# Optimization experiments

Measured on AMD Instinct MI355X. Metric: run time of the kernel, lower is better.

## Reference

```python
import jax, jax.numpy as jnp
import numpy as np
from jax import lax

L = 4096          # sequence length (timesteps)
N_ITEMS = 512     # number of items == RNN input_size (x[:,:,k] is (L, N))
HIDDEN = 256
NUM_LAYERS = 16
NUM_FEATURES = 4
OUT_SIZE = 2


def _rnn_params(key, input_size):
    """Vanilla tanh RNN params, PyTorch-style uniform(-1/sqrt(H), 1/sqrt(H))."""
    ks = jax.random.split(key, 5)
    s = 1.0 / np.sqrt(HIDDEN)
    u = lambda k, shape: jax.random.uniform(k, shape, jnp.float32, -s, s)
    return dict(
        Wih0=u(ks[0], (HIDDEN, input_size)),              # layer 0 input weights
        Wih=u(ks[1], (NUM_LAYERS - 1, HIDDEN, HIDDEN)),   # layers 1..15 input weights
        Whh=u(ks[2], (NUM_LAYERS, HIDDEN, HIDDEN)),
        bih=u(ks[3], (NUM_LAYERS, HIDDEN)),
        bhh=u(ks[4], (NUM_LAYERS, HIDDEN)),
    )


def setup_inputs() -> dict:
    key = jax.random.key(0)
    kx, k1, k2, k3 = jax.random.split(key, 4)
    x = jax.random.normal(kx, (L, N_ITEMS, NUM_FEATURES), jnp.float32)
    lp = _rnn_params(k1, N_ITEMS)    # self.low_price (used for features 0, 2, 3)
    lpv = _rnn_params(k2, N_ITEMS)   # self.low_price_vol (used for feature 1)
    kf1, kf2 = jax.random.split(k3)
    s = 1.0 / np.sqrt(HIDDEN * NUM_FEATURES)
    fc_W = jax.random.uniform(kf1, (OUT_SIZE, HIDDEN * NUM_FEATURES), jnp.float32, -s, s)
    fc_b = jax.random.uniform(kf2, (OUT_SIZE,), jnp.float32, -s, s)
    return {
        "x": x,
        "lp_Wih0": lp["Wih0"], "lp_Wih": lp["Wih"], "lp_Whh": lp["Whh"],
        "lp_bih": lp["bih"], "lp_bhh": lp["bhh"],
        "lpv_Wih0": lpv["Wih0"], "lpv_Wih": lpv["Wih"], "lpv_Whh": lpv["Whh"],
        "lpv_bih": lpv["bih"], "lpv_bhh": lpv["bhh"],
        "fc_W": fc_W, "fc_b": fc_b,
    }


def _run_rnn(seq, Wih0, Wih, Whh, bih, bhh):
    """Multi-layer vanilla tanh RNN over an unbatched (L, input_size) sequence.
    Returns the top-layer hidden state at the last timestep, shape (HIDDEN,)."""

    def step(h, x_t):  # h: (NUM_LAYERS, HIDDEN); x_t: (input_size,)
        inp = jnp.tanh(Wih0 @ x_t + bih[0] + Whh[0] @ h[0] + bhh[0])
        hs = [inp]
        for l in range(1, NUM_LAYERS):
            inp = jnp.tanh(Wih[l - 1] @ inp + bih[l] + Whh[l] @ h[l] + bhh[l])
            hs.append(inp)
        return jnp.stack(hs), None

    h0 = jnp.zeros((NUM_LAYERS, HIDDEN), seq.dtype)
    h_final, _ = lax.scan(step, h0, seq)
    return h_final[-1]


def reference(x, lp_Wih0, lp_Wih, lp_Whh, lp_bih, lp_bhh,
              lpv_Wih0, lpv_Wih, lpv_Whh, lpv_bih, lpv_bhh, fc_W, fc_b):
    lp = (lp_Wih0, lp_Wih, lp_Whh, lp_bih, lp_bhh)
    lpv = (lpv_Wih0, lpv_Wih, lpv_Whh, lpv_bih, lpv_bhh)
    # Faithful to the original (buggy) forward: low_price for features 0,2,3;
    # low_price_vol for feature 1.
    h0 = _run_rnn(x[:, :, 0], *lp)
    h1 = _run_rnn(x[:, :, 1], *lpv)
    h2 = _run_rnn(x[:, :, 2], *lp)
    h3 = _run_rnn(x[:, :, 3], *lp)
    out = jnp.concatenate([h0, h1, h2, h3])  # (4*HIDDEN,)
    return fc_W @ out + fc_b  # (OUT_SIZE,)
```

## Files before the change

kernel.cpp:

```cpp
#include <hip/hip_runtime.h>
#include <hip/hip_bf16.h>
#include <math.h>

#define SEQL   4096
#define NITEMS 512
#define HID    256
#define NLAY   16
#define QS     64
#define CHUNK  8
#define NCHUNK (SEQL / CHUNK)
#define TPB    4

typedef float f4 __attribute__((ext_vector_type(4)));

#define P_OFF   ((size_t)0)
#define H_OFF   (P_OFF + (size_t)4*SEQL*HID)
#define AP_OFF  (H_OFF + (size_t)4*NLAY*QS*HID)
#define HF_OFF  (AP_OFF + (size_t)4*NLAY*QS*HID)
#define FLAG_OFF_FLOATS (HF_OFF + (size_t)1024)
#define NFLAGS 256

__device__ __forceinline__ f4 ld_coh_f4(const float* p) {
    f4 r;
    asm volatile("global_load_dwordx4 %0, %1, off sc0 sc1" : "=v"(r) : "v"(p));
    return r;
}
__device__ __forceinline__ float ld_coh_b32(const float* p) {
    float r;
    asm volatile("global_load_dword %0, %1, off sc0 sc1" : "=v"(r) : "v"(p));
    return r;
}
__device__ __forceinline__ void st_coh_b32(float* p, float v) {
    asm volatile("global_store_dword %0, %1, off sc0 sc1" :: "v"(p), "v"(v) : "memory");
}
__device__ __forceinline__ void st_coh_u32(unsigned* p, unsigned v) {
    asm volatile("global_store_dword %0, %1, off sc0 sc1" :: "v"(p), "v"(v) : "memory");
}
__device__ __forceinline__ unsigned uload(const unsigned* p) {
    return __hip_atomic_load(p, __ATOMIC_RELAXED, __HIP_MEMORY_SCOPE_AGENT);
}

#define SBAR()  { __builtin_amdgcn_s_barrier(); __builtin_amdgcn_sched_barrier(0); }
#define LGKM0() { asm volatile("s_waitcnt lgkmcnt(0)" ::: "memory"); __builtin_amdgcn_sched_barrier(0); }
#define VMW0()  { asm volatile("s_waitcnt vmcnt(0)" ::: "memory"); __builtin_amdgcn_sched_barrier(0); }

__device__ __forceinline__ void spin_ge(const unsigned* p, unsigned target, bool* dead) {
    if (*dead) return;
    unsigned it = 0;
    while (uload(p) < target) {
        __builtin_amdgcn_s_sleep(1);
        if (++it > (1u << 20)) { *dead = true; break; }
    }
}

__device__ __forceinline__ float tanh_fast(float x) {
    return 1.f - __fdividef(2.f, __expf(2.f * x) + 1.f);
}

#define FMAC0(ACC, HB, W) \
    asm volatile("v_fmac_f32 %0, %1, %2" : "+v"(ACC) : "v"(HB), "v"(W));
#define FMACR(ACC, HB, W, I) \
    asm volatile("v_fmac_f32_dpp %0, %1, %2 row_ror:" #I " row_mask:0xf bank_mask:0xf" \
                 : "+v"(ACC) : "v"(HB), "v"(W));

#define FMAC_BLOCK(HB, WB) \
    FMAC0(acc0, HB, w[WB+0])      FMACR(acc1, HB, w[WB+1], 1)   \
    FMACR(acc2, HB, w[WB+2], 2)   FMACR(acc3, HB, w[WB+3], 3)   \
    FMACR(acc0, HB, w[WB+4], 4)   FMACR(acc1, HB, w[WB+5], 5)   \
    FMACR(acc2, HB, w[WB+6], 6)   FMACR(acc3, HB, w[WB+7], 7)   \
    FMACR(acc0, HB, w[WB+8], 8)   FMACR(acc1, HB, w[WB+9], 9)   \
    FMACR(acc2, HB, w[WB+10], 10) FMACR(acc3, HB, w[WB+11], 11) \
    FMACR(acc0, HB, w[WB+12], 12) FMACR(acc1, HB, w[WB+13], 13) \
    FMACR(acc2, HB, w[WB+14], 14) FMACR(acc3, HB, w[WB+15], 15)

__global__ __launch_bounds__(1024) void proj_kernel(
    const float* __restrict__ x, const float* __restrict__ Wlp,
    const float* __restrict__ Wlpv, float* __restrict__ P)
{
    __shared__ float xs[TPB][4][NITEMS];
    const int tid = threadIdx.x;
    const int t0 = blockIdx.x * TPB;

    #pragma unroll
    for (int tt = 0; tt < TPB; ++tt) {
        const float2* src = (const float2*)(x + (size_t)(t0 + tt) * NITEMS * 4);
        float2 v = src[tid];
        int e = 2 * tid;
        xs[tt][e & 3][e >> 2]       = v.x;
        xs[tt][(e + 1) & 3][e >> 2] = v.y;
    }
    __syncthreads();

    const int c = tid >> 8, j = tid & 255;
    const float* W = (c == 1) ? Wlpv : Wlp;
    const float4* row = (const float4*)(W + (size_t)j * NITEMS);
    float acc[TPB] = {0.f, 0.f, 0.f, 0.f};
    #pragma unroll 4
    for (int k4 = 0; k4 < NITEMS / 4; ++k4) {
        float4 w = row[k4];
        #pragma unroll
        for (int tt = 0; tt < TPB; ++tt) {
            float4 xv = *(const float4*)(&xs[tt][c][k4 * 4]);
            acc[tt] = fmaf(w.x, xv.x, fmaf(w.y, xv.y, fmaf(w.z, xv.z, fmaf(w.w, xv.w, acc[tt]))));
        }
    }
    #pragma unroll
    for (int tt = 0; tt < TPB; ++tt)
        P[((size_t)c * SEQL + (t0 + tt)) * HID + j] = acc[tt];
}

__global__ __launch_bounds__(1024) void rnn_pipe(
    const float* __restrict__ lp_Wih,  const float* __restrict__ lp_Whh,
    const float* __restrict__ lp_bih,  const float* __restrict__ lp_bhh,
    const float* __restrict__ lpv_Wih, const float* __restrict__ lpv_Whh,
    const float* __restrict__ lpv_bih, const float* __restrict__ lpv_bhh,
    const float* __restrict__ P, float* __restrict__ Hring,
    float* __restrict__ Apart, float* __restrict__ hfinal,
    unsigned* __restrict__ Hflag, unsigned* __restrict__ Aflag)
{
    __shared__ __align__(16) float part2[2][1024];
    __shared__ __align__(16) float hvec[HID];
    __shared__ __align__(16) float hstage[CHUNK * HID];
    __shared__ float ldspad[18000];

    const int b = blockIdx.x;
    if (b >= 124) return;
    const int tid = threadIdx.x;
    ldspad[tid] = 0.f;

    const int c = b / 31;
    const int r = b % 31;
    const int role = (r < NLAY) ? 0 : 1;
    const int l = (r < NLAY) ? r : (r - NLAY + 1);

    const float* Wih = (c == 1) ? lpv_Wih : lp_Wih;
    const float* Whh = (c == 1) ? lpv_Whh : lp_Whh;
    const float* bih = (c == 1) ? lpv_bih : lp_bih;
    const float* bhh = (c == 1) ? lpv_bhh : lp_bhh;

    const int j    = tid & 255;
    const int c4   = tid >> 8;
    const int lane = tid & 63;
    const int q    = lane & 15;
    const int m    = (c4 << 6) | lane;
    const int gbase = (c4 << 6) | q;
    const bool first = ((tid & 192) == 0);
    bool dead = false;

    if (role == 0) {
        const bool l0 = (l == 0);

        float w[64];
        {
            const float* Wrow = Whh + ((size_t)l * HID + j) * HID;
            #pragma unroll
            for (int bb = 0; bb < 4; ++bb)
                #pragma unroll
                for (int i = 0; i < 16; ++i)
                    w[bb * 16 + i] = Wrow[(c4 << 6) + bb * 16 + ((q - i) & 15)];
        }
        #pragma unroll
        for (int i = 0; i < 64; ++i) asm volatile("" : "+v"(w[i]));

        float bias_m = 0.f;
        if (first) bias_m = bih[l * HID + m] + bhh[l * HID + m];

        const float*    Psrc  = P + (size_t)c * SEQL * HID;
        const float*    apbuf = Apart + ((size_t)(c * NLAY + l) * QS) * HID;
        const unsigned* af    = Aflag + c * NLAY + l;
        unsigned*       myHfl = Hflag + c * NLAY + l;
        const unsigned* consA = Aflag + c * NLAY + l + 1;
        float*          Hout  = Hring + ((size_t)(c * NLAY + l) * QS) * HID;
        float*          hfin  = hfinal + (size_t)c * HID;

        float hb0 = 0.f, hb1 = 0.f, hb2 = 0.f, hb3 = 0.f;

        for (int k = 0; k < NCHUNK; ++k) {
            if (tid == 0) {
                if (!l0) spin_ge(af, (unsigned)(k + 1), &dead);
                if (l < NLAY - 1 && k >= CHUNK) spin_ge(consA, (unsigned)(k - 7), &dead);
            }
            SBAR();
            float ap8[CHUNK];
            if (first) {
                if (l0) {
                    #pragma unroll
                    for (int s = 0; s < CHUNK; ++s)
                        ap8[s] = Psrc[(size_t)(CHUNK * k + s) * HID + m];
                } else {
                    const int sbase = (k & 7) * CHUNK;
                    #pragma unroll
                    for (int s = 0; s < CHUNK; ++s)
                        ap8[s] = ld_coh_b32(apbuf + (size_t)(sbase + s) * HID + m);
                    VMW0();
                }
            }
            #pragma unroll
            for (int s = 0; s < CHUNK; ++s) {
                float acc0 = 0.f, acc1 = 0.f, acc2 = 0.f, acc3 = 0.f;
                FMAC_BLOCK(hb0, 0)
                FMAC_BLOCK(hb1, 16)
                FMAC_BLOCK(hb2, 32)
                FMAC_BLOCK(hb3, 48)
                part2[0][tid] = (acc0 + acc1) + (acc2 + acc3);
                LGKM0(); SBAR();
                if (first) {
                    const float* pb = &part2[0][0];
                    float p = pb[m] + pb[m + 256] + pb[m + 512] + pb[m + 768];
                    float h = tanh_fast(p + ap8[s] + bias_m);
                    hvec[m] = h;
                    if (l < NLAY - 1)
                        st_coh_b32(Hout + (size_t)((k & 7) * CHUNK + s) * HID + m, h);
                    else if (k == NCHUNK - 1 && s == CHUNK - 1)
                        st_coh_b32(hfin + m, h);
                    LGKM0();
                }
                SBAR();
                hb0 = hvec[gbase];      hb1 = hvec[gbase + 16];
                hb2 = hvec[gbase + 32]; hb3 = hvec[gbase + 48];
            }
            if (first) VMW0();
            SBAR();
            if (tid == 0) st_coh_u32(myHfl, (unsigned)(k + 1));
        }
    } else {
        float w[64];
        {
            const float* Wrow = Wih + ((size_t)(l - 1) * HID + j) * HID;
            #pragma unroll
            for (int bb = 0; bb < 4; ++bb)
                #pragma unroll
                for (int i = 0; i < 16; ++i)
                    w[bb * 16 + i] = Wrow[(c4 << 6) + bb * 16 + ((q - i) & 15)];
        }
        #pragma unroll
        for (int i = 0; i < 64; ++i) asm volatile("" : "+v"(w[i]));

        const float*    Hin    = Hring + ((size_t)(c * NLAY + (l - 1)) * QS) * HID;
        const unsigned* inflag = Hflag + c * NLAY + (l - 1);
        float*          Aout   = Apart + ((size_t)(c * NLAY + l) * QS) * HID;
        unsigned*       myAfl  = Aflag + c * NLAY + l;
        const unsigned* consB  = Hflag + c * NLAY + l;

        for (int k = 0; k < NCHUNK; ++k) {
            if (tid == 0) {
                spin_ge(inflag, (unsigned)(k + 1), &dead);
                if (k >= CHUNK) spin_ge(consB, (unsigned)(k - 7), &dead);
            }
            SBAR();
            if (tid < 512) {
                f4 v = ld_coh_f4(Hin + (size_t)(k & 7) * CHUNK * HID + 4 * tid);
                VMW0();
                ((f4*)hstage)[tid] = v;
                LGKM0();
            }
            SBAR();
            #pragma unroll
            for (int s = 0; s < CHUNK; ++s) {
                const float* hs = &hstage[s * HID];
                float hb0 = hs[gbase];      float hb1 = hs[gbase + 16];
                float hb2 = hs[gbase + 32]; float hb3 = hs[gbase + 48];
                float acc0 = 0.f, acc1 = 0.f, acc2 = 0.f, acc3 = 0.f;
                FMAC_BLOCK(hb0, 0)
                FMAC_BLOCK(hb1, 16)
                FMAC_BLOCK(hb2, 32)
                FMAC_BLOCK(hb3, 48)
                part2[s & 1][tid] = (acc0 + acc1) + (acc2 + acc3);
                LGKM0(); SBAR();
                if (first) {
                    const float* pb = &part2[s & 1][0];
                    float p = pb[m] + pb[m + 256] + pb[m + 512] + pb[m + 768];
                    st_coh_b32(Aout + (size_t)((k & 7) * CHUNK + s) * HID + m, p);
                }
            }
            if (first) VMW0();
            SBAR();
            if (tid == 0) st_coh_u32(myAfl, (unsigned)(k + 1));
        }
    }
}

__global__ __launch_bounds__(1024) void fc_kernel(
    const float* __restrict__ hfinal, const float* __restrict__ fcW,
    const float* __restrict__ fcb, float* __restrict__ out)
{
    __shared__ float red[1024];
    const int tid = threadIdx.x;
    float v  = hfinal[tid];
    float p0 = fcW[tid] * v;
    float p1 = fcW[1024 + tid] * v;

    red[tid] = p0; __syncthreads();
    for (int st = 512; st > 0; st >>= 1) { if (tid < st) red[tid] += red[tid + st]; __syncthreads(); }
    if (tid == 0) out[0] = red[0] + fcb[0];
    __syncthreads();
    red[tid] = p1; __syncthreads();
    for (int st = 512; st > 0; st >>= 1) { if (tid < st) red[tid] += red[tid + st]; __syncthreads(); }
    if (tid == 0) out[1] = red[0] + fcb[1];
}

extern "C" void kernel_launch(void* const* d_in, const int* in_sizes, int n_in,
                              void* d_out, int out_size, void* d_ws, size_t ws_size,
                              hipStream_t stream)
{
    (void)in_sizes; (void)n_in; (void)out_size; (void)ws_size;
    const float* x        = (const float*)d_in[0];
    const float* lp_Wih0  = (const float*)d_in[1];
    const float* lp_Wih   = (const float*)d_in[2];
    const float* lp_Whh   = (const float*)d_in[3];
    const float* lp_bih   = (const float*)d_in[4];
    const float* lp_bhh   = (const float*)d_in[5];
    const float* lpv_Wih0 = (const float*)d_in[6];
    const float* lpv_Wih  = (const float*)d_in[7];
    const float* lpv_Whh  = (const float*)d_in[8];
    const float* lpv_bih  = (const float*)d_in[9];
    const float* lpv_bhh  = (const float*)d_in[10];
    const float* fcW      = (const float*)d_in[11];
    const float* fcb      = (const float*)d_in[12];

    float* ws      = (float*)d_ws;
    float* Pbuf    = ws + P_OFF;
    float* Hring   = ws + H_OFF;
    float* Apart   = ws + AP_OFF;
    float* hfinal  = ws + HF_OFF;
    unsigned* flags = (unsigned*)(ws + FLAG_OFF_FLOATS);

    hipMemsetAsync(flags, 0, NFLAGS * sizeof(unsigned), stream);

    proj_kernel<<<SEQL / TPB, 1024, 0, stream>>>(x, lp_Wih0, lpv_Wih0, Pbuf);

    rnn_pipe<<<124, 1024, 0, stream>>>(lp_Wih, lp_Whh, lp_bih, lp_bhh,
                                       lpv_Wih, lpv_Whh, lpv_bih, lpv_bhh,
                                       Pbuf, Hring, Apart, hfinal,
                                       flags, flags + 64);

    fc_kernel<<<1, 1024, 0, stream>>>(hfinal, fcW, fcb, (float*)d_out);
}
```

Baseline: 4.705 ms.

## Broadcast hidden state via ds_bpermute to drop per-step LDS vector and barrier

In the recurrent layer blocks, every wave now computes the full reduction and tanh redundantly, so each lane holds h for its own index m. The hidden state needed by the FMAC loop is then gathered within the wave using ds_bpermute instead of going through a shared hvec buffer. This removes one block-wide barrier and an LDS round trip per timestep, and part2 is double-buffered so the next step can overwrite safely. Input-projection blocks likewise load their h values directly from global memory per lane and bpermute them, dropping the hstage staging and its barrier. The cost is redundant reduction and tanh work in all waves, more global loads, and removal of the LDS padding that had limited occupancy.

```diff
diff --git a/kernel.cpp b/kernel.cpp
--- a/kernel.cpp
+++ b/kernel.cpp
@@ -20,11 +20,6 @@
 #define FLAG_OFF_FLOATS (HF_OFF + (size_t)1024)
 #define NFLAGS 256
 
-__device__ __forceinline__ f4 ld_coh_f4(const float* p) {
-    f4 r;
-    asm volatile("global_load_dwordx4 %0, %1, off sc0 sc1" : "=v"(r) : "v"(p));
-    return r;
-}
 __device__ __forceinline__ float ld_coh_b32(const float* p) {
     float r;
     asm volatile("global_load_dword %0, %1, off sc0 sc1" : "=v"(r) : "v"(p));
@@ -72,6 +67,12 @@
     FMACR(acc2, HB, w[WB+10], 10) FMACR(acc3, HB, w[WB+11], 11) \
     FMACR(acc0, HB, w[WB+12], 12) FMACR(acc1, HB, w[WB+13], 13) \
     FMACR(acc2, HB, w[WB+14], 14) FMACR(acc3, HB, w[WB+15], 15)
+
+#define BPERM4(H) \
+    { hb0 = __int_as_float(__builtin_amdgcn_ds_bpermute(ab0, __float_as_int(H))); \
+      hb1 = __int_as_float(__builtin_amdgcn_ds_bpermute(ab1, __float_as_int(H))); \
+      hb2 = __int_as_float(__builtin_amdgcn_ds_bpermute(ab2, __float_as_int(H))); \
+      hb3 = __int_as_float(__builtin_amdgcn_ds_bpermute(ab3, __float_as_int(H))); }
 
 __global__ __launch_bounds__(1024) void proj_kernel(
     const float* __restrict__ x, const float* __restrict__ Wlp,
@@ -119,14 +120,10 @@
     unsigned* __restrict__ Hflag, unsigned* __restrict__ Aflag)
 {
     __shared__ __align__(16) float part2[2][1024];
-    __shared__ __align__(16) float hvec[HID];
-    __shared__ __align__(16) float hstage[CHUNK * HID];
-    __shared__ float ldspad[18000];
 
     const int b = blockIdx.x;
     if (b >= 124) return;
     const int tid = threadIdx.x;
-    ldspad[tid] = 0.f;
 
     const int c = b / 31;
     const int r = b % 31;
@@ -143,9 +140,13 @@
     const int lane = tid & 63;
     const int q    = lane & 15;
     const int m    = (c4 << 6) | lane;
-    const int gbase = (c4 << 6) | q;
     const bool first = ((tid & 192) == 0);
     bool dead = false;
+
+    const int ab0 = 4 * (q);
+    const int ab1 = 4 * (16 + q);
+    const int ab2 = 4 * (32 + q);
+    const int ab3 = 4 * (48 + q);
 
     if (role == 0) {
         const bool l0 = (l == 0);
@@ -162,8 +163,7 @@
         #pragma unroll
         for (int i = 0; i < 64; ++i) asm volatile("" : "+v"(w[i]));
 
-        float bias_m = 0.f;
-        if (first) bias_m = bih[l * HID + m] + bhh[l * HID + m];
+        const float bias_m = bih[l * HID + m] + bhh[l * HID + m];
 
         const float*    Psrc  = P + (size_t)c * SEQL * HID;
         const float*    apbuf = Apart + ((size_t)(c * NLAY + l) * QS) * HID;
@@ -173,7 +173,8 @@
         float*          Hout  = Hring + ((size_t)(c * NLAY + l) * QS) * HID;
         float*          hfin  = hfinal + (size_t)c * HID;
 
-        float hb0 = 0.f, hb1 = 0.f, hb2 = 0.f, hb3 = 0.f;
+        float h = 0.f;
+        float hb0, hb1, hb2, hb3;
 
         for (int k = 0; k < NCHUNK; ++k) {
             if (tid == 0) {
@@ -182,42 +183,36 @@
             }
             SBAR();
             float ap8[CHUNK];
-            if (first) {
-                if (l0) {
-                    #pragma unroll
-                    for (int s = 0; s < CHUNK; ++s)
-                        ap8[s] = Psrc[(size_t)(CHUNK * k + s) * HID + m];
-                } else {
-                    const int sbase = (k & 7) * CHUNK;
-                    #pragma unroll
-                    for (int s = 0; s < CHUNK; ++s)
-                        ap8[s] = ld_coh_b32(apbuf + (size_t)(sbase + s) * HID + m);
-                    VMW0();
-                }
+            if (l0) {
+                #pragma unroll
+                for (int s = 0; s < CHUNK; ++s)
+                    ap8[s] = Psrc[(size_t)(CHUNK * k + s) * HID + m];
+            } else {
+                const int sbase = (k & 7) * CHUNK;
+                #pragma unroll
+                for (int s = 0; s < CHUNK; ++s)
+                    ap8[s] = ld_coh_b32(apbuf + (size_t)(sbase + s) * HID + m);
+                VMW0();
             }
             #pragma unroll
             for (int s = 0; s < CHUNK; ++s) {
+                BPERM4(h);
                 float acc0 = 0.f, acc1 = 0.f, acc2 = 0.f, acc3 = 0.f;
                 FMAC_BLOCK(hb0, 0)
                 FMAC_BLOCK(hb1, 16)
                 FMAC_BLOCK(hb2, 32)
                 FMAC_BLOCK(hb3, 48)
-                part2[0][tid] = (acc0 + acc1) + (acc2 + acc3);
+                part2[s & 1][tid] = (acc0 + acc1) + (acc2 + acc3);
                 LGKM0(); SBAR();
+                const float* pb = &part2[s & 1][0];
+                float p = pb[m] + pb[m + 256] + pb[m + 512] + pb[m + 768];
+                h = tanh_fast(p + ap8[s] + bias_m);
                 if (first) {
-                    const float* pb = &part2[0][0];
-                    float p = pb[m] + pb[m + 256] + pb[m + 512] + pb[m + 768];
-                    float h = tanh_fast(p + ap8[s] + bias_m);
-                    hvec[m] = h;
                     if (l < NLAY - 1)
                         st_coh_b32(Hout + (size_t)((k & 7) * CHUNK + s) * HID + m, h);
                     else if (k == NCHUNK - 1 && s == CHUNK - 1)
                         st_coh_b32(hfin + m, h);
-                    LGKM0();
                 }
-                SBAR();
-                hb0 = hvec[gbase];      hb1 = hvec[gbase + 16];
-                hb2 = hvec[gbase + 32]; hb3 = hvec[gbase + 48];
             }
             if (first) VMW0();
             SBAR();
@@ -242,24 +237,25 @@
         unsigned*       myAfl  = Aflag + c * NLAY + l;
         const unsigned* consB  = Hflag + c * NLAY + l;
 
+        float hb0, hb1, hb2, hb3;
+
         for (int k = 0; k < NCHUNK; ++k) {
             if (tid == 0) {
                 spin_ge(inflag, (unsigned)(k + 1), &dead);
                 if (k >= CHUNK) spin_ge(consB, (unsigned)(k - 7), &dead);
             }
             SBAR();
-            if (tid < 512) {
-                f4 v = ld_coh_f4(Hin + (size_t)(k & 7) * CHUNK * HID + 4 * tid);
+            float h8[CHUNK];
+            {
+                const float* hbase = Hin + (size_t)(k & 7) * CHUNK * HID + m;
+                #pragma unroll
+                for (int s = 0; s < CHUNK; ++s)
+                    h8[s] = ld_coh_b32(hbase + (size_t)s * HID);
                 VMW0();
-                ((f4*)hstage)[tid] = v;
-                LGKM0();
-            }
-            SBAR();
+            }
             #pragma unroll
             for (int s = 0; s < CHUNK; ++s) {
-                const float* hs = &hstage[s * HID];
-                float hb0 = hs[gbase];      float hb1 = hs[gbase + 16];
-                float hb2 = hs[gbase + 32]; float hb3 = hs[gbase + 48];
+                BPERM4(h8[s]);
                 float acc0 = 0.f, acc1 = 0.f, acc2 = 0.f, acc3 = 0.f;
                 FMAC_BLOCK(hb0, 0)
                 FMAC_BLOCK(hb1, 16)
```

After: 4.286 ms. 1.1x faster.
